# Kernel optimization log

Hardware: AMD Instinct MI355X
Metric: run time of the kernel (lower is better)

## Reference

```python
import jax, jax.numpy as jnp
import numpy as np

E, M, K, I, TOPK = 8, 4096, 2048, 1408, 2
N = 2 * I  # gated: w1 produces [gate, up]


def setup_inputs() -> dict:
    key = jax.random.key(0)
    k1, k2, k3, k4, k5 = jax.random.split(key, 5)
    hidden_states = jax.random.normal(k1, (M, K), dtype=jnp.float32)
    w1 = jax.random.normal(k2, (E, N, K), dtype=jnp.float32) * 0.02
    w2 = jax.random.normal(k3, (E, K, I), dtype=jnp.float32) * 0.02
    raw = jax.random.uniform(k4, (M, TOPK), dtype=jnp.float32)
    topk_weights = raw / jnp.sum(raw, axis=-1, keepdims=True)  # router probs
    topk_ids = jax.random.randint(k5, (M, TOPK), 0, E, dtype=jnp.int32)
    return {
        "hidden_states": hidden_states,
        "w1": w1,
        "w2": w2,
        "topk_weights": topk_weights,
        "topk_ids": topk_ids,
    }


def reference(hidden_states, w1, w2, topk_weights, topk_ids):
    # MoE: permute -> grouped GEMM1 -> silu_and_mul -> grouped GEMM2 -> unpermute+reduce.
    # Dense-per-expert formulation (math-equivalent to grouped GEMM over routed tokens).
    # GEMM1: [E, M, N]
    h1 = jnp.einsum("mk,enk->emn", hidden_states, w1)
    gate, up = h1[..., :I], h1[..., I:]
    act = jax.nn.silu(gate) * up  # silu_and_mul, [E, M, I]
    # GEMM2: [E, M, K]
    y = jnp.einsum("emi,eki->emk", act, w2)
    # Unpermute: gather each token's topk expert outputs, apply router weights, reduce.
    y_tok = jnp.transpose(y, (1, 0, 2))  # [M, E, K]
    sel = jnp.take_along_axis(y_tok, topk_ids[:, :, None].astype(jnp.int32), axis=1)  # [M, topk, K]
    out = jnp.sum(sel * topk_weights[:, :, None], axis=1)  # [M, K]
    return out
```

## Files before the change

kernel.cpp:

```cpp
#include <hip/hip_runtime.h>
#include <hip/hip_bf16.h>
#include <stdint.h>

#define EXPERTS 8
#define MTOK 4096
#define KDIM 2048
#define IDIM 1408
#define NDIM 2816
#define CAP  8192

typedef __attribute__((ext_vector_type(8))) short bf16x8;
typedef __attribute__((ext_vector_type(4))) float f32x4;

__device__ __forceinline__ unsigned short f2bf(float x) {
    unsigned u = __float_as_uint(x);
    u = u + 0x7fffu + ((u >> 16) & 1u);
    return (unsigned short)(u >> 16);
}

__device__ __forceinline__ void gload16(const void* g, void* l) {
    __builtin_amdgcn_global_load_lds(
        (const __attribute__((address_space(1))) void*)g,
        (__attribute__((address_space(3))) void*)l, 16, 0, 0);
}

__global__ void __launch_bounds__(256) conv_bf16(const float* __restrict__ src,
                                                 unsigned short* __restrict__ dst, int n4) {
    int i = blockIdx.x * 256 + threadIdx.x;
    int st = gridDim.x * 256;
    for (; i < n4; i += st) {
        float4 v = reinterpret_cast<const float4*>(src)[i];
        ushort4 r;
        r.x = f2bf(v.x); r.y = f2bf(v.y); r.z = f2bf(v.z); r.w = f2bf(v.w);
        reinterpret_cast<ushort4*>(dst)[i] = r;
    }
}

__global__ void __launch_bounds__(256) router(const float* __restrict__ tw,
                                              const int* __restrict__ ids,
                                              int* __restrict__ tok, float* __restrict__ wgt,
                                              int* __restrict__ cnt) {
    int m = blockIdx.x * 256 + threadIdx.x;
    if (m >= MTOK) return;
#pragma unroll
    for (int t = 0; t < 2; t++) {
        int e = ids[m * 2 + t];
        int slot = atomicAdd(&cnt[e], 1);
        tok[e * CAP + slot] = m;
        wgt[e * CAP + slot] = tw[m * 2 + t];
    }
}

__global__ void scan_off(const int* __restrict__ cnt, int* __restrict__ off) {
    if (threadIdx.x == 0) {
        int s = 0;
        for (int e = 0; e < EXPERTS; e++) { off[e] = s; s += cnt[e]; }
    }
}


__global__ void __launch_bounds__(256) gemm1_silu(
    const unsigned short* __restrict__ hsb,
    const unsigned short* __restrict__ w1b,
    const int* __restrict__ tok,
    const int* __restrict__ cnt,
    const int* __restrict__ off,
    unsigned short* __restrict__ act) {
    const int bid = blockIdx.x;
    const int e = bid & 7;
    const int j = bid >> 3;
    const int rb = j / 22;
    const int cb = j - rb * 22;
    const int cnt_e = cnt[e];
    if (rb * 128 >= cnt_e) return;
    const int off_e = off[e];

    __shared__ unsigned short As[128 * 32];
    __shared__ unsigned short Bs[128 * 32];
    __shared__ int toks[128];

    const int tid = threadIdx.x;
    const int w = tid >> 6, lane = tid & 63;
    if (tid < 128) {
        int slot = rb * 128 + tid;
        toks[tid] = (slot < cnt_e) ? tok[e * CAP + slot] : 0;
    }
    __syncthreads();

    const int o0 = w * 1024 + lane * 16;
    const int row0 = o0 >> 6, g0 = ((o0 >> 4) & 3) ^ ((row0 >> 1) & 3);
    const int o1 = 4096 + o0;
    const int row1 = o1 >> 6, g1 = ((o1 >> 4) & 3) ^ ((row1 >> 1) & 3);

    const int G0 = row0 >> 4, G1 = row1 >> 4;
    const size_t w1base = (size_t)e * NDIM * KDIM;
    const int wrow0 = ((G0 & 1) ? IDIM : 0) + cb * 64 + (G0 >> 1) * 16 + (row0 & 15);
    const int wrow1 = ((G1 & 1) ? IDIM : 0) + cb * 64 + (G1 >> 1) * 16 + (row1 & 15);

    const int wr = w >> 1, wc = w & 1;
    const int l16 = lane & 15, lg = lane >> 4;

    f32x4 acc[4][4];
#pragma unroll
    for (int m = 0; m < 4; m++)
#pragma unroll
        for (int n = 0; n < 4; n++) acc[m][n] = {0.f, 0.f, 0.f, 0.f};

    char* Ab = (char*)As;
    char* Bb = (char*)Bs;
    const size_t srcA0 = (size_t)toks[row0] * KDIM + g0 * 8;
    const size_t srcA1 = (size_t)toks[row1] * KDIM + g1 * 8;
    const size_t srcB0 = w1base + (size_t)wrow0 * KDIM + g0 * 8;
    const size_t srcB1 = w1base + (size_t)wrow1 * KDIM + g1 * 8;

    for (int kt = 0; kt < KDIM / 32; ++kt) {
        const int kof = kt * 32;
        gload16(hsb + srcA0 + kof, Ab + w * 1024);
        gload16(hsb + srcA1 + kof, Ab + 4096 + w * 1024);
        gload16(w1b + srcB0 + kof, Bb + w * 1024);
        gload16(w1b + srcB1 + kof, Bb + 4096 + w * 1024);
        __syncthreads();

        bf16x8 a[4], b[4];
#pragma unroll
        for (int m = 0; m < 4; m++) {
            int r = wr * 64 + m * 16 + l16;
            a[m] = *reinterpret_cast<bf16x8*>(Ab + r * 64 + ((lg ^ ((r >> 1) & 3)) * 16));
        }
#pragma unroll
        for (int n = 0; n < 4; n++) {
            int r = wc * 64 + n * 16 + l16;
            b[n] = *reinterpret_cast<bf16x8*>(Bb + r * 64 + ((lg ^ ((r >> 1) & 3)) * 16));
        }
#pragma unroll
        for (int m = 0; m < 4; m++)
#pragma unroll
            for (int n = 0; n < 4; n++)
                acc[m][n] = __builtin_amdgcn_mfma_f32_16x16x32_bf16(a[m], b[n], acc[m][n], 0, 0, 0);
        __syncthreads();
    }

#pragma unroll
    for (int m = 0; m < 4; m++) {
#pragma unroll
        for (int np = 0; np < 2; np++) {
            f32x4 g4 = acc[m][np * 2];
            f32x4 u4 = acc[m][np * 2 + 1];
            int icol = cb * 64 + (wc * 2 + np) * 16 + l16;
#pragma unroll
            for (int j2 = 0; j2 < 4; j2++) {
                int grow = rb * 128 + wr * 64 + m * 16 + lg * 4 + j2;
                if (grow < cnt_e) {
                    float gt = g4[j2], up = u4[j2];
                    float s = gt / (1.f + __expf(-gt));
                    act[(size_t)(off_e + grow) * IDIM + icol] = f2bf(s * up);
                }
            }
        }
    }
}

__global__ void __launch_bounds__(256) gemm2_scatter(
    const unsigned short* __restrict__ act,
    const unsigned short* __restrict__ w2b,
    const int* __restrict__ tok,
    const float* __restrict__ wgt,
    const int* __restrict__ cnt,
    const int* __restrict__ off,
    float* __restrict__ out) {
    const int bid = blockIdx.x;
    const int e = bid & 7;
    const int j = bid >> 3;
    const int rb = j >> 4;
    const int cb = j & 15;
    const int cnt_e = cnt[e];
    if (rb * 128 >= cnt_e) return;
    const int off_e = off[e];

    __shared__ unsigned short As[128 * 32];
    __shared__ unsigned short Bs[128 * 32];
    __shared__ int toks[128];
    __shared__ float wgts[128];

    const int tid = threadIdx.x;
    const int w = tid >> 6, lane = tid & 63;
    if (tid < 128) {
        int slot = rb * 128 + tid;
        bool v = slot < cnt_e;
        toks[tid] = v ? tok[e * CAP + slot] : 0;
        wgts[tid] = v ? wgt[e * CAP + slot] : 0.f;
    }
    __syncthreads();

    const int o0 = w * 1024 + lane * 16;
    const int row0 = o0 >> 6, g0 = ((o0 >> 4) & 3) ^ ((row0 >> 1) & 3);
    const int o1 = 4096 + o0;
    const int row1 = o1 >> 6, g1 = ((o1 >> 4) & 3) ^ ((row1 >> 1) & 3);

    const int s0 = rb * 128 + row0, s1 = rb * 128 + row1;
    const size_t pa0 = (size_t)(off_e + (s0 < cnt_e ? s0 : 0)) * IDIM + g0 * 8;
    const size_t pa1 = (size_t)(off_e + (s1 < cnt_e ? s1 : 0)) * IDIM + g1 * 8;
    const size_t w2base = (size_t)e * KDIM * IDIM;
    const size_t pb0 = w2base + (size_t)(cb * 128 + row0) * IDIM + g0 * 8;
    const size_t pb1 = w2base + (size_t)(cb * 128 + row1) * IDIM + g1 * 8;

    const int wr = w >> 1, wc = w & 1;
    const int l16 = lane & 15, lg = lane >> 4;

    f32x4 acc[4][4];
#pragma unroll
    for (int m = 0; m < 4; m++)
#pragma unroll
        for (int n = 0; n < 4; n++) acc[m][n] = {0.f, 0.f, 0.f, 0.f};

    char* Ab = (char*)As;
    char* Bb = (char*)Bs;

    for (int kt = 0; kt < IDIM / 32; ++kt) {
        const int kof = kt * 32;
        gload16(act + pa0 + kof, Ab + w * 1024);
        gload16(act + pa1 + kof, Ab + 4096 + w * 1024);
        gload16(w2b + pb0 + kof, Bb + w * 1024);
        gload16(w2b + pb1 + kof, Bb + 4096 + w * 1024);
        __syncthreads();

        bf16x8 a[4], b[4];
#pragma unroll
        for (int m = 0; m < 4; m++) {
            int r = wr * 64 + m * 16 + l16;
            a[m] = *reinterpret_cast<bf16x8*>(Ab + r * 64 + ((lg ^ ((r >> 1) & 3)) * 16));
        }
#pragma unroll
        for (int n = 0; n < 4; n++) {
            int r = wc * 64 + n * 16 + l16;
            b[n] = *reinterpret_cast<bf16x8*>(Bb + r * 64 + ((lg ^ ((r >> 1) & 3)) * 16));
        }
#pragma unroll
        for (int m = 0; m < 4; m++)
#pragma unroll
            for (int n = 0; n < 4; n++)
                acc[m][n] = __builtin_amdgcn_mfma_f32_16x16x32_bf16(a[m], b[n], acc[m][n], 0, 0, 0);
        __syncthreads();
    }

#pragma unroll
    for (int m = 0; m < 4; m++) {
#pragma unroll
        for (int n = 0; n < 4; n++) {
            int kcol = cb * 128 + wc * 64 + n * 16 + l16;
#pragma unroll
            for (int j2 = 0; j2 < 4; j2++) {
                int lrow = wr * 64 + m * 16 + lg * 4 + j2;
                if (rb * 128 + lrow < cnt_e) {
                    atomicAdd(&out[(size_t)toks[lrow] * KDIM + kcol],
                              wgts[lrow] * acc[m][n][j2]);
                }
            }
        }
    }
}

extern "C" void kernel_launch(void* const* d_in, const int* in_sizes, int n_in,
                              void* d_out, int out_size, void* d_ws, size_t ws_size,
                              hipStream_t stream) {
    const float* hs  = (const float*)d_in[0];
    const float* w1  = (const float*)d_in[1];
    const float* w2  = (const float*)d_in[2];
    const float* tw  = (const float*)d_in[3];
    const int*   ids = (const int*)d_in[4];
    float* out = (float*)d_out;

    char* ws = (char*)d_ws;
    unsigned short* w1b  = (unsigned short*)(ws);
    unsigned short* w2b  = (unsigned short*)(ws + 92274688ull);
    unsigned short* hsb  = (unsigned short*)(ws + 138412032ull);
    unsigned short* actb = (unsigned short*)(ws + 155189248ull);
    int*   tokb = (int*)  (ws + 178257920ull);
    float* wgtb = (float*)(ws + 178520064ull);
    int*   cntb = (int*)  (ws + 178782208ull);
    int*   offb = (int*)  (ws + 178782240ull);

    hipMemsetAsync(d_out, 0, (size_t)MTOK * KDIM * sizeof(float), stream);
    hipMemsetAsync(cntb, 0, 64, stream);

    conv_bf16<<<4096, 256, 0, stream>>>(w1, w1b, EXPERTS * NDIM * KDIM / 4);
    conv_bf16<<<2048, 256, 0, stream>>>(w2, w2b, EXPERTS * KDIM * IDIM / 4);
    conv_bf16<<<1024, 256, 0, stream>>>(hs, hsb, MTOK * KDIM / 4);

    router<<<MTOK / 256, 256, 0, stream>>>(tw, ids, tokb, wgtb, cntb);
    scan_off<<<1, 64, 0, stream>>>(cntb, offb);

    gemm1_silu<<<dim3(22 * 64 * 8, 1, 1), 256, 0, stream>>>(hsb, w1b, tokb, cntb, offb, actb);
    gemm2_scatter<<<dim3(16 * 64 * 8, 1, 1), 256, 0, stream>>>(actb, w2b, tokb, wgtb, cntb, offb, out);
}
```

Before: 383.3 us.

## Fuse fp32-to-bf16 conversion into GEMM loads with register double buffering

Removes the standalone conversion kernels for weights and hidden states and instead loads fp32 directly inside both GEMMs, converting to bf16 in registers before writing swizzled LDS tiles. Adds a two-stage register/LDS double buffer with manual waitcnt and barriers to overlap global loads with MFMA work. This eliminates a full extra pass over the weights, at the cost of doubling global bytes per tile fetch, extra VALU conversion work, and higher register pressure.

```diff
diff --git a/kernel.cpp b/kernel.cpp
--- a/kernel.cpp
+++ b/kernel.cpp
@@ -18,22 +18,13 @@
     return (unsigned short)(u >> 16);
 }
 
-__device__ __forceinline__ void gload16(const void* g, void* l) {
-    __builtin_amdgcn_global_load_lds(
-        (const __attribute__((address_space(1))) void*)g,
-        (__attribute__((address_space(3))) void*)l, 16, 0, 0);
-}
-
-__global__ void __launch_bounds__(256) conv_bf16(const float* __restrict__ src,
-                                                 unsigned short* __restrict__ dst, int n4) {
-    int i = blockIdx.x * 256 + threadIdx.x;
-    int st = gridDim.x * 256;
-    for (; i < n4; i += st) {
-        float4 v = reinterpret_cast<const float4*>(src)[i];
-        ushort4 r;
-        r.x = f2bf(v.x); r.y = f2bf(v.y); r.z = f2bf(v.z); r.w = f2bf(v.w);
-        reinterpret_cast<ushort4*>(dst)[i] = r;
-    }
+__device__ __forceinline__ bf16x8 cvt8(float4 x, float4 y) {
+    bf16x8 r;
+    r[0] = (short)f2bf(x.x); r[1] = (short)f2bf(x.y);
+    r[2] = (short)f2bf(x.z); r[3] = (short)f2bf(x.w);
+    r[4] = (short)f2bf(y.x); r[5] = (short)f2bf(y.y);
+    r[6] = (short)f2bf(y.z); r[7] = (short)f2bf(y.w);
+    return r;
 }
 
 __global__ void __launch_bounds__(256) router(const float* __restrict__ tw,
@@ -59,9 +50,9 @@
 }
 
 
-__global__ void __launch_bounds__(256) gemm1_silu(
-    const unsigned short* __restrict__ hsb,
-    const unsigned short* __restrict__ w1b,
+__global__ void __launch_bounds__(256, 2) gemm1_silu(
+    const float* __restrict__ hs,
+    const float* __restrict__ w1,
     const int* __restrict__ tok,
     const int* __restrict__ cnt,
     const int* __restrict__ off,
@@ -74,9 +65,9 @@
     const int cnt_e = cnt[e];
     if (rb * 128 >= cnt_e) return;
     const int off_e = off[e];
-
-    __shared__ unsigned short As[128 * 32];
-    __shared__ unsigned short Bs[128 * 32];
+    const int NT = KDIM / 32;
+
+    __shared__ __align__(16) char smem[32768];
     __shared__ int toks[128];
 
     const int tid = threadIdx.x;
@@ -87,18 +78,35 @@
     }
     __syncthreads();
 
-    const int o0 = w * 1024 + lane * 16;
-    const int row0 = o0 >> 6, g0 = ((o0 >> 4) & 3) ^ ((row0 >> 1) & 3);
-    const int o1 = 4096 + o0;
-    const int row1 = o1 >> 6, g1 = ((o1 >> 4) & 3) ^ ((row1 >> 1) & 3);
-
-    const int G0 = row0 >> 4, G1 = row1 >> 4;
-    const size_t w1base = (size_t)e * NDIM * KDIM;
-    const int wrow0 = ((G0 & 1) ? IDIM : 0) + cb * 64 + (G0 >> 1) * 16 + (row0 & 15);
-    const int wrow1 = ((G1 & 1) ? IDIM : 0) + cb * 64 + (G1 >> 1) * 16 + (row1 & 15);
+    const int rA0 = tid >> 2, gA = tid & 3;
+    const int rA1 = 64 + rA0;
+    const size_t srcA0 = (size_t)toks[rA0] * KDIM + gA * 8;
+    const size_t srcA1 = (size_t)toks[rA1] * KDIM + gA * 8;
+    const int dA0 = rA0 * 64 + ((gA ^ ((rA0 >> 1) & 3)) * 16);
+    const int dA1 = rA1 * 64 + ((gA ^ ((rA1 >> 1) & 3)) * 16);
+
+    const size_t w1base = (size_t)e * (size_t)NDIM * KDIM;
+    const int G0 = rA0 >> 4, G1 = rA1 >> 4;
+    const int wrow0 = ((G0 & 1) ? IDIM : 0) + cb * 64 + (G0 >> 1) * 16 + (rA0 & 15);
+    const int wrow1 = ((G1 & 1) ? IDIM : 0) + cb * 64 + (G1 >> 1) * 16 + (rA1 & 15);
+    const size_t srcB0 = w1base + (size_t)wrow0 * KDIM + gA * 8;
+    const size_t srcB1 = w1base + (size_t)wrow1 * KDIM + gA * 8;
+    const int dB0 = 8192 + dA0;
+    const int dB1 = 8192 + dA1;
 
     const int wr = w >> 1, wc = w & 1;
     const int l16 = lane & 15, lg = lane >> 4;
+    int aoff[4], boff[4];
+#pragma unroll
+    for (int m = 0; m < 4; m++) {
+        int r = wr * 64 + m * 16 + l16;
+        aoff[m] = r * 64 + ((lg ^ ((r >> 1) & 3)) * 16);
+    }
+#pragma unroll
+    for (int n = 0; n < 4; n++) {
+        int r = wc * 64 + n * 16 + l16;
+        boff[n] = 8192 + r * 64 + ((lg ^ ((r >> 1) & 3)) * 16);
+    }
 
     f32x4 acc[4][4];
 #pragma unroll
@@ -106,39 +114,51 @@
 #pragma unroll
         for (int n = 0; n < 4; n++) acc[m][n] = {0.f, 0.f, 0.f, 0.f};
 
-    char* Ab = (char*)As;
-    char* Bb = (char*)Bs;
-    const size_t srcA0 = (size_t)toks[row0] * KDIM + g0 * 8;
-    const size_t srcA1 = (size_t)toks[row1] * KDIM + g1 * 8;
-    const size_t srcB0 = w1base + (size_t)wrow0 * KDIM + g0 * 8;
-    const size_t srcB1 = w1base + (size_t)wrow1 * KDIM + g1 * 8;
-
-    for (int kt = 0; kt < KDIM / 32; ++kt) {
-        const int kof = kt * 32;
-        gload16(hsb + srcA0 + kof, Ab + w * 1024);
-        gload16(hsb + srcA1 + kof, Ab + 4096 + w * 1024);
-        gload16(w1b + srcB0 + kof, Bb + w * 1024);
-        gload16(w1b + srcB1 + kof, Bb + 4096 + w * 1024);
-        __syncthreads();
-
-        bf16x8 a[4], b[4];
-#pragma unroll
-        for (int m = 0; m < 4; m++) {
-            int r = wr * 64 + m * 16 + l16;
-            a[m] = *reinterpret_cast<bf16x8*>(Ab + r * 64 + ((lg ^ ((r >> 1) & 3)) * 16));
-        }
-#pragma unroll
-        for (int n = 0; n < 4; n++) {
-            int r = wc * 64 + n * 16 + l16;
-            b[n] = *reinterpret_cast<bf16x8*>(Bb + r * 64 + ((lg ^ ((r >> 1) & 3)) * 16));
-        }
-#pragma unroll
-        for (int m = 0; m < 4; m++)
-#pragma unroll
-            for (int n = 0; n < 4; n++)
-                acc[m][n] = __builtin_amdgcn_mfma_f32_16x16x32_bf16(a[m], b[n], acc[m][n], 0, 0, 0);
-        __syncthreads();
-    }
+    struct RegT { float4 a00, a01, a10, a11, b00, b01, b10, b11; };
+    RegT Ra, Rb;
+
+#define LOADR1(R, t) { const int ko = (t) * 32; \
+    R.a00 = *(const float4*)(hs + srcA0 + ko);     R.a01 = *(const float4*)(hs + srcA0 + ko + 4); \
+    R.a10 = *(const float4*)(hs + srcA1 + ko);     R.a11 = *(const float4*)(hs + srcA1 + ko + 4); \
+    R.b00 = *(const float4*)(w1 + srcB0 + ko);     R.b01 = *(const float4*)(w1 + srcB0 + ko + 4); \
+    R.b10 = *(const float4*)(w1 + srcB1 + ko);     R.b11 = *(const float4*)(w1 + srcB1 + ko + 4); }
+#define CVW1(R, base) { \
+    *(bf16x8*)(smem + (base) + dA0) = cvt8(R.a00, R.a01); \
+    *(bf16x8*)(smem + (base) + dA1) = cvt8(R.a10, R.a11); \
+    *(bf16x8*)(smem + (base) + dB0) = cvt8(R.b00, R.b01); \
+    *(bf16x8*)(smem + (base) + dB1) = cvt8(R.b10, R.b11); }
+#define FRAG1(base) { bf16x8 af[4], bf[4]; \
+    _Pragma("unroll") for (int m = 0; m < 4; m++) af[m] = *(const bf16x8*)(smem + (base) + aoff[m]); \
+    _Pragma("unroll") for (int n = 0; n < 4; n++) bf[n] = *(const bf16x8*)(smem + (base) + boff[n]); \
+    _Pragma("unroll") for (int m = 0; m < 4; m++) \
+    _Pragma("unroll") for (int n = 0; n < 4; n++) \
+        acc[m][n] = __builtin_amdgcn_mfma_f32_16x16x32_bf16(af[m], bf[n], acc[m][n], 0, 0, 0); }
+
+    LOADR1(Ra, 0);
+#pragma unroll 1
+    for (int kt = 0; kt < NT; kt += 2) {
+        if (kt + 1 < NT) { LOADR1(Rb, kt + 1); asm volatile("s_waitcnt vmcnt(8)" ::: "memory"); }
+        else             { asm volatile("s_waitcnt vmcnt(0)" ::: "memory"); }
+        __builtin_amdgcn_sched_barrier(0);
+        CVW1(Ra, 0);
+        asm volatile("s_waitcnt lgkmcnt(0)" ::: "memory");
+        __builtin_amdgcn_sched_barrier(0);
+        __builtin_amdgcn_s_barrier();
+        __builtin_amdgcn_sched_barrier(0);
+        FRAG1(0);
+        if (kt + 2 < NT) { LOADR1(Ra, kt + 2); asm volatile("s_waitcnt vmcnt(8)" ::: "memory"); }
+        else             { asm volatile("s_waitcnt vmcnt(0)" ::: "memory"); }
+        __builtin_amdgcn_sched_barrier(0);
+        CVW1(Rb, 16384);
+        asm volatile("s_waitcnt lgkmcnt(0)" ::: "memory");
+        __builtin_amdgcn_sched_barrier(0);
+        __builtin_amdgcn_s_barrier();
+        __builtin_amdgcn_sched_barrier(0);
+        FRAG1(16384);
+    }
+#undef LOADR1
+#undef CVW1
+#undef FRAG1
 
 #pragma unroll
     for (int m = 0; m < 4; m++) {
@@ -160,9 +180,9 @@
     }
 }
 
-__global__ void __launch_bounds__(256) gemm2_scatter(
+__global__ void __launch_bounds__(256, 2) gemm2_scatter(
     const unsigned short* __restrict__ act,
-    const unsigned short* __restrict__ w2b,
+    const float* __restrict__ w2,
     const int* __restrict__ tok,
     const float* __restrict__ wgt,
     const int* __restrict__ cnt,
@@ -176,9 +196,9 @@
     const int cnt_e = cnt[e];
     if (rb * 128 >= cnt_e) return;
     const int off_e = off[e];
-
-    __shared__ unsigned short As[128 * 32];
-    __shared__ unsigned short Bs[128 * 32];
+    const int NT = IDIM / 32;
+
+    __shared__ __align__(16) char smem[32768];
     __shared__ int toks[128];
     __shared__ float wgts[128];
 
@@ -192,20 +212,33 @@
     }
     __syncthreads();
 
-    const int o0 = w * 1024 + lane * 16;
-    const int row0 = o0 >> 6, g0 = ((o0 >> 4) & 3) ^ ((row0 >> 1) & 3);
-    const int o1 = 4096 + o0;
-    const int row1 = o1 >> 6, g1 = ((o1 >> 4) & 3) ^ ((row1 >> 1) & 3);
-
-    const int s0 = rb * 128 + row0, s1 = rb * 128 + row1;
-    const size_t pa0 = (size_t)(off_e + (s0 < cnt_e ? s0 : 0)) * IDIM + g0 * 8;
-    const size_t pa1 = (size_t)(off_e + (s1 < cnt_e ? s1 : 0)) * IDIM + g1 * 8;
-    const size_t w2base = (size_t)e * KDIM * IDIM;
-    const size_t pb0 = w2base + (size_t)(cb * 128 + row0) * IDIM + g0 * 8;
-    const size_t pb1 = w2base + (size_t)(cb * 128 + row1) * IDIM + g1 * 8;
+    const int rA0 = tid >> 2, gA = tid & 3;
+    const int rA1 = 64 + rA0;
+    const int s0 = rb * 128 + rA0, s1 = rb * 128 + rA1;
+    const size_t srcA0 = (size_t)(off_e + (s0 < cnt_e ? s0 : 0)) * IDIM + gA * 8;
+    const size_t srcA1 = (size_t)(off_e + (s1 < cnt_e ? s1 : 0)) * IDIM + gA * 8;
+    const int dA0 = rA0 * 64 + ((gA ^ ((rA0 >> 1) & 3)) * 16);
+    const int dA1 = rA1 * 64 + ((gA ^ ((rA1 >> 1) & 3)) * 16);
+
+    const size_t w2base = (size_t)e * (size_t)KDIM * IDIM;
+    const size_t srcB0 = w2base + (size_t)(cb * 128 + rA0) * IDIM + gA * 8;
+    const size_t srcB1 = w2base + (size_t)(cb * 128 + rA1) * IDIM + gA * 8;
+    const int dB0 = 8192 + dA0;
+    const int dB1 = 8192 + dA1;
 
     const int wr = w >> 1, wc = w & 1;
     const int l16 = lane & 15, lg = lane >> 4;
+    int aoff[4], boff[4];
+#pragma unroll
+    for (int m = 0; m < 4; m++) {
+        int r = wr * 64 + m * 16 + l16;
+        aoff[m] = r * 64 + ((lg ^ ((r >> 1) & 3)) * 16);
+    }
+#pragma unroll
+    for (int n = 0; n < 4; n++) {
+        int r = wc * 64 + n * 16 + l16;
+        boff[n] = 8192 + r * 64 + ((lg ^ ((r >> 1) & 3)) * 16);
+    }
 
     f32x4 acc[4][4];
 #pragma unroll
@@ -213,35 +246,51 @@
 #pragma unroll
         for (int n = 0; n < 4; n++) acc[m][n] = {0.f, 0.f, 0.f, 0.f};
 
-    char* Ab = (char*)As;
-    char* Bb = (char*)Bs;
-
-    for (int kt = 0; kt < IDIM / 32; ++kt) {
-        const int kof = kt * 32;
-        gload16(act + pa0 + kof, Ab + w * 1024);
-        gload16(act + pa1 + kof, Ab + 4096 + w * 1024);
-        gload16(w2b + pb0 + kof, Bb + w * 1024);
-        gload16(w2b + pb1 + kof, Bb + 4096 + w * 1024);
-        __syncthreads();
-
-        bf16x8 a[4], b[4];
-#pragma unroll
-        for (int m = 0; m < 4; m++) {
-            int r = wr * 64 + m * 16 + l16;
-            a[m] = *reinterpret_cast<bf16x8*>(Ab + r * 64 + ((lg ^ ((r >> 1) & 3)) * 16));
-        }
-#pragma unroll
-        for (int n = 0; n < 4; n++) {
-            int r = wc * 64 + n * 16 + l16;
-            b[n] = *reinterpret_cast<bf16x8*>(Bb + r * 64 + ((lg ^ ((r >> 1) & 3)) * 16));
-        }
-#pragma unroll
-        for (int m = 0; m < 4; m++)
-#pragma unroll
-            for (int n = 0; n < 4; n++)
-                acc[m][n] = __builtin_amdgcn_mfma_f32_16x16x32_bf16(a[m], b[n], acc[m][n], 0, 0, 0);
-        __syncthreads();
-    }
+    struct RegT2 { uint4 aa0, aa1; float4 b00, b01, b10, b11; };
+    RegT2 Ra, Rb;
+
+#define LOADR2(R, t) { const int ko = (t) * 32; \
+    R.aa0 = *(const uint4*)(act + srcA0 + ko); \
+    R.aa1 = *(const uint4*)(act + srcA1 + ko); \
+    R.b00 = *(const float4*)(w2 + srcB0 + ko); R.b01 = *(const float4*)(w2 + srcB0 + ko + 4); \
+    R.b10 = *(const float4*)(w2 + srcB1 + ko); R.b11 = *(const float4*)(w2 + srcB1 + ko + 4); }
+#define CVW2(R, base) { \
+    *(uint4*)(smem + (base) + dA0) = R.aa0; \
+    *(uint4*)(smem + (base) + dA1) = R.aa1; \
+    *(bf16x8*)(smem + (base) + dB0) = cvt8(R.b00, R.b01); \
+    *(bf16x8*)(smem + (base) + dB1) = cvt8(R.b10, R.b11); }
+#define FRAG2(base) { bf16x8 af[4], bf[4]; \
+    _Pragma("unroll") for (int m = 0; m < 4; m++) af[m] = *(const bf16x8*)(smem + (base) + aoff[m]); \
+    _Pragma("unroll") for (int n = 0; n < 4; n++) bf[n] = *(const bf16x8*)(smem + (base) + boff[n]); \
+    _Pragma("unroll") for (int m = 0; m < 4; m++) \
+    _Pragma("unroll") for (int n = 0; n < 4; n++) \
+        acc[m][n] = __builtin_amdgcn_mfma_f32_16x16x32_bf16(af[m], bf[n], acc[m][n], 0, 0, 0); }
+
+    LOADR2(Ra, 0);
+#pragma unroll 1
+    for (int kt = 0; kt < NT; kt += 2) {
+        if (kt + 1 < NT) { LOADR2(Rb, kt + 1); asm volatile("s_waitcnt vmcnt(6)" ::: "memory"); }
+        else             { asm volatile("s_waitcnt vmcnt(0)" ::: "memory"); }
+        __builtin_amdgcn_sched_barrier(0);
+        CVW2(Ra, 0);
+        asm volatile("s_waitcnt lgkmcnt(0)" ::: "memory");
+        __builtin_amdgcn_sched_barrier(0);
+        __builtin_amdgcn_s_barrier();
+        __builtin_amdgcn_sched_barrier(0);
+        FRAG2(0);
+        if (kt + 2 < NT) { LOADR2(Ra, kt + 2); asm volatile("s_waitcnt vmcnt(6)" ::: "memory"); }
+        else             { asm volatile("s_waitcnt vmcnt(0)" ::: "memory"); }
+        __builtin_amdgcn_sched_barrier(0);
+        CVW2(Rb, 16384);
+        asm volatile("s_waitcnt lgkmcnt(0)" ::: "memory");
+        __builtin_amdgcn_sched_barrier(0);
+        __builtin_amdgcn_s_barrier();
+        __builtin_amdgcn_sched_barrier(0);
+        FRAG2(16384);
+    }
+#undef LOADR2
+#undef CVW2
+#undef FRAG2
 
 #pragma unroll
     for (int m = 0; m < 4; m++) {
@@ -271,25 +320,18 @@
     float* out = (float*)d_out;
 
     char* ws = (char*)d_ws;
-    unsigned short* w1b  = (unsigned short*)(ws);
-    unsigned short* w2b  = (unsigned short*)(ws + 92274688ull);
-    unsigned short* hsb  = (unsigned short*)(ws + 138412032ull);
-    unsigned short* actb = (unsigned short*)(ws + 155189248ull);
-    int*   tokb = (int*)  (ws + 178257920ull);
-    float* wgtb = (float*)(ws + 178520064ull);
-    int*   cntb = (int*)  (ws + 178782208ull);
-    int*   offb = (int*)  (ws + 178782240ull);
+    unsigned short* actb = (unsigned short*)(ws);
+    int*   tokb = (int*)  (ws + 23068672ull);
+    float* wgtb = (float*)(ws + 23330816ull);
+    int*   cntb = (int*)  (ws + 23592960ull);
+    int*   offb = (int*)  (ws + 23592992ull);
 
     hipMemsetAsync(d_out, 0, (size_t)MTOK * KDIM * sizeof(float), stream);
     hipMemsetAsync(cntb, 0, 64, stream);
 
-    conv_bf16<<<4096, 256, 0, stream>>>(w1, w1b, EXPERTS * NDIM * KDIM / 4);
-    conv_bf16<<<2048, 256, 0, stream>>>(w2, w2b, EXPERTS * KDIM * IDIM / 4);
-    conv_bf16<<<1024, 256, 0, stream>>>(hs, hsb, MTOK * KDIM / 4);
-
     router<<<MTOK / 256, 256, 0, stream>>>(tw, ids, tokb, wgtb, cntb);
     scan_off<<<1, 64, 0, stream>>>(cntb, offb);
 
-    gemm1_silu<<<dim3(22 * 64 * 8, 1, 1), 256, 0, stream>>>(hsb, w1b, tokb, cntb, offb, actb);
-    gemm2_scatter<<<dim3(16 * 64 * 8, 1, 1), 256, 0, stream>>>(actb, w2b, tokb, wgtb, cntb, offb, out);
-}
+    gemm1_silu<<<dim3(22 * 64 * 8, 1, 1), 256, 0, stream>>>(hs, w1, tokb, cntb, offb, actb);
+    gemm2_scatter<<<dim3(16 * 64 * 8, 1, 1), 256, 0, stream>>>(actb, w2, tokb, wgtb, cntb, offb, out);
+}
```

Measured after the change: 472.0 us. 23.1% more time.

## Triple-buffer LDS with async global-to-LDS prefetch in both MoE GEMMs

Applied to the files above, without the earlier changes.

Replaces the single-buffered load/sync/compute loop in both grouped GEMM kernels with a three-stage LDS ring, issuing global_load_lds for tile t+2 while computing tile t. Manual vmcnt waits and one barrier per iteration replace two __syncthreads, and MFMA sections get raised wave priority. Launch bounds now request 3 blocks per CU. The change targets exposed global load latency, at the cost of 48KB of LDS per block, which may limit occupancy.

```diff
diff --git a/kernel.cpp b/kernel.cpp
--- a/kernel.cpp
+++ b/kernel.cpp
@@ -59,7 +59,7 @@
 }
 
 
-__global__ void __launch_bounds__(256) gemm1_silu(
+__global__ void __launch_bounds__(256, 3) gemm1_silu(
     const unsigned short* __restrict__ hsb,
     const unsigned short* __restrict__ w1b,
     const int* __restrict__ tok,
@@ -74,9 +74,9 @@
     const int cnt_e = cnt[e];
     if (rb * 128 >= cnt_e) return;
     const int off_e = off[e];
-
-    __shared__ unsigned short As[128 * 32];
-    __shared__ unsigned short Bs[128 * 32];
+    const int NT = KDIM / 32;
+
+    __shared__ __align__(16) char smem[49152];
     __shared__ int toks[128];
 
     const int tid = threadIdx.x;
@@ -97,48 +97,73 @@
     const int wrow0 = ((G0 & 1) ? IDIM : 0) + cb * 64 + (G0 >> 1) * 16 + (row0 & 15);
     const int wrow1 = ((G1 & 1) ? IDIM : 0) + cb * 64 + (G1 >> 1) * 16 + (row1 & 15);
 
-    const int wr = w >> 1, wc = w & 1;
-    const int l16 = lane & 15, lg = lane >> 4;
-
-    f32x4 acc[4][4];
-#pragma unroll
-    for (int m = 0; m < 4; m++)
-#pragma unroll
-        for (int n = 0; n < 4; n++) acc[m][n] = {0.f, 0.f, 0.f, 0.f};
-
-    char* Ab = (char*)As;
-    char* Bb = (char*)Bs;
     const size_t srcA0 = (size_t)toks[row0] * KDIM + g0 * 8;
     const size_t srcA1 = (size_t)toks[row1] * KDIM + g1 * 8;
     const size_t srcB0 = w1base + (size_t)wrow0 * KDIM + g0 * 8;
     const size_t srcB1 = w1base + (size_t)wrow1 * KDIM + g1 * 8;
 
-    for (int kt = 0; kt < KDIM / 32; ++kt) {
-        const int kof = kt * 32;
-        gload16(hsb + srcA0 + kof, Ab + w * 1024);
-        gload16(hsb + srcA1 + kof, Ab + 4096 + w * 1024);
-        gload16(w1b + srcB0 + kof, Bb + w * 1024);
-        gload16(w1b + srcB1 + kof, Bb + 4096 + w * 1024);
-        __syncthreads();
-
-        bf16x8 a[4], b[4];
-#pragma unroll
-        for (int m = 0; m < 4; m++) {
-            int r = wr * 64 + m * 16 + l16;
-            a[m] = *reinterpret_cast<bf16x8*>(Ab + r * 64 + ((lg ^ ((r >> 1) & 3)) * 16));
-        }
-#pragma unroll
-        for (int n = 0; n < 4; n++) {
-            int r = wc * 64 + n * 16 + l16;
-            b[n] = *reinterpret_cast<bf16x8*>(Bb + r * 64 + ((lg ^ ((r >> 1) & 3)) * 16));
-        }
+    const int wr = w >> 1, wc = w & 1;
+    const int l16 = lane & 15, lg = lane >> 4;
+    int aoff[4], boff[4];
+#pragma unroll
+    for (int m = 0; m < 4; m++) {
+        int r = wr * 64 + m * 16 + l16;
+        aoff[m] = r * 64 + ((lg ^ ((r >> 1) & 3)) * 16);
+    }
+#pragma unroll
+    for (int n = 0; n < 4; n++) {
+        int r = wc * 64 + n * 16 + l16;
+        boff[n] = 8192 + r * 64 + ((lg ^ ((r >> 1) & 3)) * 16);
+    }
+
+    f32x4 acc[4][4];
+#pragma unroll
+    for (int m = 0; m < 4; m++)
+#pragma unroll
+        for (int n = 0; n < 4; n++) acc[m][n] = {0.f, 0.f, 0.f, 0.f};
+
+#define STG1(t, base) { const int kof_ = (t) * 32; char* b_ = smem + (base); \
+    gload16(hsb + srcA0 + kof_, b_ + w * 1024); \
+    gload16(hsb + srcA1 + kof_, b_ + 4096 + w * 1024); \
+    gload16(w1b + srcB0 + kof_, b_ + 8192 + w * 1024); \
+    gload16(w1b + srcB1 + kof_, b_ + 12288 + w * 1024); }
+
+    STG1(0, 0); STG1(1, 16384);
+    asm volatile("s_waitcnt vmcnt(4)" ::: "memory");
+    __builtin_amdgcn_sched_barrier(0);
+    __builtin_amdgcn_s_barrier();
+
+    int sl_t = 0;
+    int sl_p = 32768;
+
+#pragma unroll 1
+    for (int t = 0; t < NT; ++t) {
+        if (t + 2 < NT) STG1(t + 2, sl_p);
+        __builtin_amdgcn_sched_barrier(0);
+
+        const char* db = smem + sl_t;
+        bf16x8 af[4], bf[4];
+#pragma unroll
+        for (int m = 0; m < 4; m++) af[m] = *(const bf16x8*)(db + aoff[m]);
+#pragma unroll
+        for (int n = 0; n < 4; n++) bf[n] = *(const bf16x8*)(db + boff[n]);
+        __builtin_amdgcn_s_setprio(1);
 #pragma unroll
         for (int m = 0; m < 4; m++)
 #pragma unroll
             for (int n = 0; n < 4; n++)
-                acc[m][n] = __builtin_amdgcn_mfma_f32_16x16x32_bf16(a[m], b[n], acc[m][n], 0, 0, 0);
-        __syncthreads();
-    }
+                acc[m][n] = __builtin_amdgcn_mfma_f32_16x16x32_bf16(af[m], bf[n], acc[m][n], 0, 0, 0);
+        __builtin_amdgcn_s_setprio(0);
+        __builtin_amdgcn_sched_barrier(0);
+        if (t + 2 < NT)      { asm volatile("s_waitcnt vmcnt(4)" ::: "memory"); }
+        else if (t + 1 < NT) { asm volatile("s_waitcnt vmcnt(0)" ::: "memory"); }
+        __builtin_amdgcn_sched_barrier(0);
+        __builtin_amdgcn_s_barrier();
+
+        sl_t += 16384; if (sl_t == 49152) sl_t = 0;
+        sl_p += 16384; if (sl_p == 49152) sl_p = 0;
+    }
+#undef STG1
 
 #pragma unroll
     for (int m = 0; m < 4; m++) {
@@ -160,7 +185,7 @@
     }
 }
 
-__global__ void __launch_bounds__(256) gemm2_scatter(
+__global__ void __launch_bounds__(256, 3) gemm2_scatter(
     const unsigned short* __restrict__ act,
     const unsigned short* __restrict__ w2b,
     const int* __restrict__ tok,
@@ -176,9 +201,9 @@
     const int cnt_e = cnt[e];
     if (rb * 128 >= cnt_e) return;
     const int off_e = off[e];
-
-    __shared__ unsigned short As[128 * 32];
-    __shared__ unsigned short Bs[128 * 32];
+    const int NT = IDIM / 32;
+
+    __shared__ __align__(16) char smem[49152];
     __shared__ int toks[128];
     __shared__ float wgts[128];
 
@@ -206,6 +231,17 @@
 
     const int wr = w >> 1, wc = w & 1;
     const int l16 = lane & 15, lg = lane >> 4;
+    int aoff[4], boff[4];
+#pragma unroll
+    for (int m = 0; m < 4; m++) {
+        int r = wr * 64 + m * 16 + l16;
+        aoff[m] = r * 64 + ((lg ^ ((r >> 1) & 3)) * 16);
+    }
+#pragma unroll
+    for (int n = 0; n < 4; n++) {
+        int r = wc * 64 + n * 16 + l16;
+        boff[n] = 8192 + r * 64 + ((lg ^ ((r >> 1) & 3)) * 16);
+    }
 
     f32x4 acc[4][4];
 #pragma unroll
@@ -213,35 +249,48 @@
 #pragma unroll
         for (int n = 0; n < 4; n++) acc[m][n] = {0.f, 0.f, 0.f, 0.f};
 
-    char* Ab = (char*)As;
-    char* Bb = (char*)Bs;
-
-    for (int kt = 0; kt < IDIM / 32; ++kt) {
-        const int kof = kt * 32;
-        gload16(act + pa0 + kof, Ab + w * 1024);
-        gload16(act + pa1 + kof, Ab + 4096 + w * 1024);
-        gload16(w2b + pb0 + kof, Bb + w * 1024);
-        gload16(w2b + pb1 + kof, Bb + 4096 + w * 1024);
-        __syncthreads();
-
-        bf16x8 a[4], b[4];
-#pragma unroll
-        for (int m = 0; m < 4; m++) {
-            int r = wr * 64 + m * 16 + l16;
-            a[m] = *reinterpret_cast<bf16x8*>(Ab + r * 64 + ((lg ^ ((r >> 1) & 3)) * 16));
-        }
-#pragma unroll
-        for (int n = 0; n < 4; n++) {
-            int r = wc * 64 + n * 16 + l16;
-            b[n] = *reinterpret_cast<bf16x8*>(Bb + r * 64 + ((lg ^ ((r >> 1) & 3)) * 16));
-        }
+#define STG2(t, base) { const int kof_ = (t) * 32; char* b_ = smem + (base); \
+    gload16(act + pa0 + kof_, b_ + w * 1024); \
+    gload16(act + pa1 + kof_, b_ + 4096 + w * 1024); \
+    gload16(w2b + pb0 + kof_, b_ + 8192 + w * 1024); \
+    gload16(w2b + pb1 + kof_, b_ + 12288 + w * 1024); }
+
+    STG2(0, 0); STG2(1, 16384);
+    asm volatile("s_waitcnt vmcnt(4)" ::: "memory");
+    __builtin_amdgcn_sched_barrier(0);
+    __builtin_amdgcn_s_barrier();
+
+    int sl_t = 0;
+    int sl_p = 32768;
+
+#pragma unroll 1
+    for (int t = 0; t < NT; ++t) {
+        if (t + 2 < NT) STG2(t + 2, sl_p);
+        __builtin_amdgcn_sched_barrier(0);
+
+        const char* db = smem + sl_t;
+        bf16x8 af[4], bf[4];
+#pragma unroll
+        for (int m = 0; m < 4; m++) af[m] = *(const bf16x8*)(db + aoff[m]);
+#pragma unroll
+        for (int n = 0; n < 4; n++) bf[n] = *(const bf16x8*)(db + boff[n]);
+        __builtin_amdgcn_s_setprio(1);
 #pragma unroll
         for (int m = 0; m < 4; m++)
 #pragma unroll
             for (int n = 0; n < 4; n++)
-                acc[m][n] = __builtin_amdgcn_mfma_f32_16x16x32_bf16(a[m], b[n], acc[m][n], 0, 0, 0);
-        __syncthreads();
-    }
+                acc[m][n] = __builtin_amdgcn_mfma_f32_16x16x32_bf16(af[m], bf[n], acc[m][n], 0, 0, 0);
+        __builtin_amdgcn_s_setprio(0);
+        __builtin_amdgcn_sched_barrier(0);
+        if (t + 2 < NT)      { asm volatile("s_waitcnt vmcnt(4)" ::: "memory"); }
+        else if (t + 1 < NT) { asm volatile("s_waitcnt vmcnt(0)" ::: "memory"); }
+        __builtin_amdgcn_sched_barrier(0);
+        __builtin_amdgcn_s_barrier();
+
+        sl_t += 16384; if (sl_t == 49152) sl_t = 0;
+        sl_p += 16384; if (sl_p == 49152) sl_p = 0;
+    }
+#undef STG2
 
 #pragma unroll
     for (int m = 0; m < 4; m++) {
```

New measurement: 393.7 us. 1.03x slower.
